# Kernel tuning notes

Measured on AMD Instinct MI355X. Metric: run time of the kernel, lower is better.

## Reference

```python
import jax, jax.numpy as jnp
import numpy as np


def setup_inputs() -> dict:
    key = jax.random.key(0)
    k1, k2, k3, k4 = jax.random.split(key, 4)
    B, N, dim, heads, dim_head = 4, 1025, 768, 12, 64
    inner = heads * dim_head
    x = jax.random.normal(k1, (B, N, dim), dtype=jnp.float32)
    # binary occlusion mask over the N-1 patch tokens (CLS handled inside forward)
    mask = (jax.random.uniform(k2, (B, N - 1, dim)) > 0.5).astype(jnp.float32)
    w_qkv = jax.random.normal(k3, (inner * 3, dim), dtype=jnp.float32) * 0.02
    w_out = jax.random.normal(k4, (dim, inner), dtype=jnp.float32) * 0.02
    b_out = jnp.zeros((dim,), dtype=jnp.float32)
    return {"x": x, "mask": mask, "w_qkv": w_qkv, "w_out": w_out, "b_out": b_out, "heads": heads}


def reference(x, mask, w_qkv, w_out, b_out, heads):
    B, N, dim = x.shape
    inner = w_qkv.shape[0] // 3
    d = inner // heads
    scale = d ** -0.5

    def split_heads(t):  # [B, n, h*d] -> [B, h, n, d]
        return t.reshape(B, t.shape[1], heads, d).transpose(0, 2, 1, 3)

    qkv = x @ w_qkv.T  # [B, N, 3*inner]
    q, k, v = map(split_heads, jnp.split(qkv, 3, axis=-1))

    # --- mask propagation (torch.no_grad block) ---
    mask_sg = jax.lax.stop_gradient(mask)
    qkv_m = mask_sg @ jax.lax.stop_gradient(jnp.abs(w_qkv)).T  # [B, N-1, 3*inner]

    def norm_mask(t):
        t = split_heads(t)  # [B, h, N-1, d]
        t = t / (1e-6 + jnp.max(t, axis=2, keepdims=True))
        return jnp.concatenate([jnp.ones_like(t[:, :, :1]), t], axis=2)  # [B, h, N, d]

    q_m, k_m, v_m = map(norm_mask, jnp.split(qkv_m, 3, axis=-1))
    updated = (jnp.mean(mask_sg, axis=-1, keepdims=True) > 0.0).astype(x.dtype)  # [B, N-1, 1]
    updated = jnp.concatenate([jnp.ones_like(updated[:, :1]), updated], axis=1)  # [B, N, 1]

    # --- masked attention ---
    dots = jnp.einsum('bhnd,bhmd->bhnm', q * q_m, k * k_m) * scale
    attn = jax.nn.softmax(dots, axis=-1)
    out = jnp.einsum('bhnm,bhmd->bhnd', attn, v_m * v)
    out = out.transpose(0, 2, 1, 3).reshape(B, N, inner) * updated
    out = out @ w_out.T + b_out

    # --- mask output propagation (no grad) ---
    m = jax.lax.stop_gradient(jnp.einsum('bhnm,bhmd->bhnd', attn, v_m))
    m = m.transpose(0, 2, 1, 3).reshape(B, N, inner) * updated
    m = m @ jax.lax.stop_gradient(jnp.abs(w_out)).T
    return (out, m[:, 1:])
```

## Files before the change

### kernel.cpp

```cpp
#include <hip/hip_runtime.h>
#include <cmath>

#define TPB 256

static const int NTOK  = 1025;
static const int DIM   = 768;
static const int HEADS = 12;
static const int QK3   = 2304;
static const int ROWS  = 4 * NTOK;
static const int MROWS = 4 * (NTOK - 1);
static const int MPAD  = 4224;
static const int NPAD  = 1088;
static const size_t OUT0 = (size_t)ROWS * DIM;
static const size_t APLANE = (size_t)MPAD * DIM;

static const size_t OFF_QKV16  = 0;
static const size_t OFF_QKVM16 = 4800000;
static const size_t OFF_QE     = 9600000;
static const size_t OFF_KF     = 11300000;
static const size_t OFF_VF     = 13000000;
static const size_t OFF_ABF    = 16400000;
static const size_t OFF_WQ     = 19700000;
static const size_t OFF_WO     = 21500000;
static const size_t OFF_CMAX   = 22100000;
static const size_t OFF_UPD    = 22110000;

typedef __attribute__((ext_vector_type(8))) short short8;
typedef __attribute__((ext_vector_type(4))) float f32x4;

__device__ __forceinline__ unsigned short f2bf(float f) {
    union { float f; unsigned int u; } c; c.f = f;
    unsigned int u = c.u + 0x7fffu + ((c.u >> 16) & 1u);
    return (unsigned short)(u >> 16);
}
__device__ __forceinline__ float bf2f(unsigned short u) {
    union { unsigned int u; float f; } c; c.u = (unsigned int)u << 16;
    return c.f;
}
__device__ __forceinline__ unsigned int cvtpk(float a, float b) {
    unsigned int r;
    asm("v_cvt_pk_bf16_f32 %0, %1, %2" : "=v"(r) : "v"(a), "v"(b));
    return r;
}
__device__ __forceinline__ void gl_lds16(const unsigned short* g, unsigned short* l) {
    __builtin_amdgcn_global_load_lds(
        (const __attribute__((address_space(1))) unsigned int*)g,
        (__attribute__((address_space(3))) unsigned int*)l, 16, 0, 0);
}

__global__ __launch_bounds__(TPB)
void k_cvt(const float* __restrict__ x, const float* __restrict__ mask,
           const float* __restrict__ wqkv, const float* __restrict__ wout,
           unsigned short* __restrict__ Abf, unsigned short* __restrict__ Wq,
           unsigned short* __restrict__ Wo, float* __restrict__ upd,
           float* __restrict__ cmax)
{
    const int z = blockIdx.z;
    if (z == 4) {
        const int bx = blockIdx.x;
        if (bx < 1025) {
            const int w = threadIdx.x >> 6, lane = threadIdx.x & 63;
            const int r = bx * 4 + w;
            if (r >= ROWS) return;
            const int b = r / NTOK, n = r % NTOK;
            float res = 1.f;
            if (n > 0) {
                const float* p = mask + (size_t)(b * (NTOK - 1) + (n - 1)) * DIM;
                float s = 0.f;
                for (int i = lane; i < DIM; i += 64) s += p[i];
#pragma unroll
                for (int off = 32; off > 0; off >>= 1) s += __shfl_xor(s, off, 64);
                res = (s > 0.f) ? 1.f : 0.f;
            }
            if (lane == 0) upd[r] = res;
        } else if (bx < 1034) {
            const int i4 = (bx - 1025) * 256 + threadIdx.x;
            *(float4*)(cmax + (size_t)i4 * 4) = (float4){0.f, 0.f, 0.f, 0.f};
        }
        return;
    }
    const size_t idx = ((size_t)blockIdx.x * TPB + threadIdx.x) * 8;
    unsigned short o[8] __attribute__((aligned(16)));
    if (z <= 1) {
        if (idx >= APLANE) return;
        const int row = (int)(idx / DIM);
        const int M = z ? MROWS : ROWS;
        const float* src = z ? mask : x;
        if (row < M) {
            float a[8];
            *(float4*)&a[0] = *(const float4*)(src + idx);
            *(float4*)&a[4] = *(const float4*)(src + idx + 4);
#pragma unroll
            for (int i = 0; i < 8; ++i) o[i] = f2bf(a[i]);
        } else {
#pragma unroll
            for (int i = 0; i < 8; ++i) o[i] = 0;
        }
        *(short8*)(Abf + (size_t)z * APLANE + idx) = *(short8*)o;
    } else {
        const size_t tot = (z == 2) ? (size_t)QK3 * DIM : (size_t)DIM * DIM;
        if (idx >= tot) return;
        const float* src = (z == 2) ? wqkv : wout;
        unsigned short* dst = (z == 2) ? Wq : Wo;
        float a[8];
        *(float4*)&a[0] = *(const float4*)(src + idx);
        *(float4*)&a[4] = *(const float4*)(src + idx + 4);
        unsigned short oa[8] __attribute__((aligned(16)));
#pragma unroll
        for (int i = 0; i < 8; ++i) { o[i] = f2bf(a[i]); oa[i] = f2bf(fabsf(a[i])); }
        *(short8*)(dst + idx) = *(short8*)o;
        *(short8*)(dst + tot + idx) = *(short8*)oa;
    }
}

__global__ __launch_bounds__(TPB)
void k_gemm_qkv_mfma(const unsigned short* __restrict__ Abf,
                     const unsigned short* __restrict__ Wq,
                     unsigned short* __restrict__ qkv16,
                     unsigned short* __restrict__ qkvm16,
                     float* __restrict__ cmax)
{
    const int bid = blockIdx.x;
    const int xcd = bid & 7, rr = bid >> 3;
    const int id = (xcd < 4) ? (xcd * 149 + rr) : (596 + (xcd - 4) * 148 + rr);
    const int z = id / 594;
    const int rem = id - z * 594;
    const int by = rem / 18, bx = rem - by * 18;
    const int rowT = by * 128, colT = bx * 128;
    if (z == 1 && rowT >= MROWS) return;
    const unsigned short* A = Abf + (size_t)z * APLANE;
    const unsigned short* B = Wq + (size_t)z * QK3 * DIM;

    __shared__ unsigned short As[2][128 * 64];
    __shared__ unsigned short Bs[2][128 * 64];

    const int t = threadIdx.x;
    const int w = t >> 6, lane = t & 63, l15 = lane & 15, quad = lane >> 4;
    const int wm = (w & 1) * 64, wn = (w >> 1) * 64;

    auto stage = [&](int buf, int k0) {
#pragma unroll
        for (int p = 0; p < 4; ++p) {
            const int i = p * 256 + t;
            const int row = i >> 3, ch = i & 7;
            const int gc = k0 + ((ch ^ (row & 7)) << 3);
            gl_lds16(A + (size_t)(rowT + row) * DIM + gc, As[buf] + (size_t)i * 8);
            gl_lds16(B + (size_t)(colT + row) * DIM + gc, Bs[buf] + (size_t)i * 8);
        }
    };

    f32x4 acc[4][4];
#pragma unroll
    for (int i = 0; i < 4; ++i)
#pragma unroll
        for (int j = 0; j < 4; ++j) acc[i][j] = (f32x4){0.f, 0.f, 0.f, 0.f};

    stage(0, 0);
#pragma clang loop unroll(disable)
    for (int kt = 0; kt < 12; ++kt) {
        const int cur = kt & 1;
        if (kt < 11) {
            stage(cur ^ 1, (kt + 1) * 64);
            asm volatile("s_waitcnt vmcnt(8)" ::: "memory");
        } else {
            asm volatile("s_waitcnt vmcnt(0)" ::: "memory");
        }
        __builtin_amdgcn_s_barrier();
        __builtin_amdgcn_sched_barrier(0);
        const unsigned short* as = As[cur];
        const unsigned short* bs = Bs[cur];
        short8 fa[2][4], fb[2][4];
#pragma unroll
        for (int kk = 0; kk < 2; ++kk) {
            const int rc = ((kk * 4 + quad) ^ (l15 & 7)) << 3;
#pragma unroll
            for (int mi = 0; mi < 4; ++mi) {
                fa[kk][mi] = *(const short8*)(as + (wm + mi * 16 + l15) * 64 + rc);
                fb[kk][mi] = *(const short8*)(bs + (wn + mi * 16 + l15) * 64 + rc);
            }
        }
        __builtin_amdgcn_s_setprio(1);
#pragma unroll
        for (int kk = 0; kk < 2; ++kk)
#pragma unroll
            for (int mi = 0; mi < 4; ++mi)
#pragma unroll
                for (int ni = 0; ni < 4; ++ni)
                    acc[mi][ni] = __builtin_amdgcn_mfma_f32_16x16x32_bf16(fa[kk][mi], fb[kk][ni], acc[mi][ni], 0, 0, 0);
        __builtin_amdgcn_s_setprio(0);
        asm volatile("s_waitcnt lgkmcnt(0)" ::: "memory");
        __builtin_amdgcn_s_barrier();
    }

    float cm[4] = {0.f, 0.f, 0.f, 0.f};
#pragma unroll
    for (int mi = 0; mi < 4; ++mi)
#pragma unroll
        for (int ni = 0; ni < 4; ++ni) {
            const int col = colT + wn + ni * 16 + l15;
#pragma unroll
            for (int r = 0; r < 4; ++r) {
                const int row = rowT + wm + mi * 16 + quad * 4 + r;
                const float v = acc[mi][ni][r];
                if (z == 0) {
                    if (row < ROWS) qkv16[(size_t)row * QK3 + col] = f2bf(v);
                } else {
                    qkvm16[(size_t)row * QK3 + col] = f2bf(v);
                    cm[ni] = fmaxf(cm[ni], v);
                }
            }
        }
    if (z == 1) {
        const int bb = rowT >> 10;
#pragma unroll
        for (int ni = 0; ni < 4; ++ni) {
            float m = cm[ni];
            m = fmaxf(m, __shfl_xor(m, 16, 64));
            m = fmaxf(m, __shfl_xor(m, 32, 64));
            if (quad == 0)
                atomicMax((int*)&cmax[bb * QK3 + colT + wn + ni * 16 + l15], __float_as_int(m));
        }
    }
}

__global__ __launch_bounds__(TPB)
void k_prep(const unsigned short* __restrict__ qkv16,
            const unsigned short* __restrict__ qkvm16,
            const float* __restrict__ cmax, unsigned short* __restrict__ qe,
            unsigned short* __restrict__ kfrag, unsigned short* __restrict__ vfrag)
{
    __shared__ unsigned short Vt_l[128 * 66];
    const int t = threadIdx.x;
    const int nt = blockIdx.x, h = blockIdx.y, b = blockIdx.z;
    const int bh = b * HEADS + h;
    const int nl = t >> 2, ds0 = (t & 3) * 16;
    const int n = nt * 64 + nl;
    const bool valid = n < NTOK;
    const int col0 = h * 64 + ds0;

    unsigned short q16[16] __attribute__((aligned(16))) = {0};
    unsigned short k16[16] __attribute__((aligned(16))) = {0};
    unsigned short v16[16] __attribute__((aligned(16))) = {0};
    unsigned short qm16[16] __attribute__((aligned(16)));
    unsigned short km16[16] __attribute__((aligned(16)));
    unsigned short vm16[16] __attribute__((aligned(16)));
    float cq[16], ck[16], cv[16];

    const bool useM = valid && (n > 0);
    if (valid) {
        const size_t br = (size_t)(b * NTOK + n) * QK3 + col0;
        *(short8*)&q16[0] = *(const short8*)(qkv16 + br);
        *(short8*)&q16[8] = *(const short8*)(qkv16 + br + 8);
        *(short8*)&k16[0] = *(const short8*)(qkv16 + br + 768);
        *(short8*)&k16[8] = *(const short8*)(qkv16 + br + 776);
        *(short8*)&v16[0] = *(const short8*)(qkv16 + br + 1536);
        *(short8*)&v16[8] = *(const short8*)(qkv16 + br + 1544);
    }
    if (useM) {
        const size_t mr = (size_t)(b * 1024 + (n - 1)) * QK3 + col0;
        *(short8*)&qm16[0] = *(const short8*)(qkvm16 + mr);
        *(short8*)&qm16[8] = *(const short8*)(qkvm16 + mr + 8);
        *(short8*)&km16[0] = *(const short8*)(qkvm16 + mr + 768);
        *(short8*)&km16[8] = *(const short8*)(qkvm16 + mr + 776);
        *(short8*)&vm16[0] = *(const short8*)(qkvm16 + mr + 1536);
        *(short8*)&vm16[8] = *(const short8*)(qkvm16 + mr + 1544);
        const int cb = b * QK3 + col0;
#pragma unroll
        for (int i = 0; i < 4; ++i) {
            *(float4*)&cq[i * 4] = *(const float4*)(cmax + cb + i * 4);
            *(float4*)&ck[i * 4] = *(const float4*)(cmax + cb + 768 + i * 4);
            *(float4*)&cv[i * 4] = *(const float4*)(cmax + cb + 1536 + i * 4);
        }
    }

    unsigned short oq[16] __attribute__((aligned(16)));
    unsigned short ok[16] __attribute__((aligned(16)));
#pragma unroll
    for (int idx = 0; idx < 16; ++idx) {
        const float qm = useM ? bf2f(qm16[idx]) / (1e-6f + cq[idx]) : 1.f;
        const float km = useM ? bf2f(km16[idx]) / (1e-6f + ck[idx]) : 1.f;
        const float vm = valid ? (useM ? bf2f(vm16[idx]) / (1e-6f + cv[idx]) : 1.f) : 0.f;
        oq[idx] = f2bf(bf2f(q16[idx]) * qm * 0.18033688f);
        ok[idx] = f2bf(bf2f(k16[idx]) * km);
        const int d = ds0 + idx;
        Vt_l[d * 66 + nl]        = f2bf(bf2f(v16[idx]) * vm);
        Vt_l[(64 + d) * 66 + nl] = f2bf(vm);
    }
    {
        unsigned short* qp = qe + ((size_t)bh * NPAD + n) * 64 + ds0;
        *(short8*)qp       = *(short8*)oq;
        *(short8*)(qp + 8) = *(short8*)(oq + 8);
    }
    {
        const int nc = nl >> 4, l15 = nl & 15;
        const int kk = ds0 >> 5, qb = (ds0 & 31) >> 3;
        unsigned short* kp = kfrag + (((size_t)bh * 17 + nt) * 8 + kk * 4 + nc) * 512;
        *(short8*)(kp + ((size_t)(qb * 16 + l15)) * 8)       = *(short8*)ok;
        *(short8*)(kp + ((size_t)((qb + 1) * 16 + l15)) * 8) = *(short8*)(ok + 8);
    }
    __syncthreads();
    const int c = t >> 1, nh = (t & 1) * 32;
    unsigned short ov[32] __attribute__((aligned(16)));
#pragma unroll
    for (int i = 0; i < 32; ++i) ov[i] = Vt_l[c * 66 + nh + i];
    const int c8 = c >> 4, l15v = c & 15, kkv = nh >> 5;
    unsigned short* vp = vfrag + (((size_t)bh * 17 + nt) * 16 + c8 * 2 + kkv) * 512 + (size_t)l15v * 8;
#pragma unroll
    for (int qd = 0; qd < 4; ++qd)
        *(short8*)(vp + (size_t)qd * 128) = *(short8*)(ov + qd * 8);
}

__global__ __launch_bounds__(64, 2)
void k_attn(const unsigned short* __restrict__ qe, const unsigned short* __restrict__ kfrag,
            const unsigned short* __restrict__ vfrag, const float* __restrict__ upd,
            unsigned short* __restrict__ ab2)
{
    const int flat = blockIdx.y * 33 + blockIdx.x;
    const int d2 = (flat & 7) * 198 + (flat >> 3);
    const int bh = d2 / 33, qt = d2 - bh * 33;
    const int b = bh / HEADS, h = bh - b * HEADS;
    const int lane = threadIdx.x;
    const int l15 = lane & 15, quad = lane >> 4;
    const int q0 = qt * 32;

    short8 qf[2][2];
#pragma unroll
    for (int j = 0; j < 2; ++j) {
        const unsigned short* qp = qe + ((size_t)bh * NPAD + q0 + j * 16 + l15) * 64 + (quad << 3);
        qf[j][0] = *(const short8*)qp;
        qf[j][1] = *(const short8*)(qp + 32);
    }
    const int pA = (quad & 1) * 32 + l15;
    const int pB = pA + 16;
    const bool lo32 = (lane < 32);

    const unsigned short* kb = kfrag + (size_t)bh * (17 * 8 * 512) + (size_t)lane * 8;
    const unsigned short* vb = vfrag + (size_t)bh * (17 * 16 * 512) + (size_t)lane * 8;

    short8 kf[8], vf[16];
#pragma unroll
    for (int g = 0; g < 8; ++g) kf[g] = *(const short8*)(kb + g * 512);
#pragma unroll
    for (int g = 0; g < 16; ++g) vf[g] = *(const short8*)(vb + g * 512);

    f32x4 acc[2][8];
    float lac[2] = {0.f, 0.f};
#pragma unroll
    for (int j = 0; j < 2; ++j)
#pragma unroll
        for (int g = 0; g < 8; ++g) acc[j][g] = (f32x4){0.f, 0.f, 0.f, 0.f};

    const float EC = 14.4269504f;

#pragma clang loop unroll(disable)
    for (int kt = 0; kt < 17; ++kt) {
        f32x4 s[2][4];
        __builtin_amdgcn_s_setprio(1);
#pragma unroll
        for (int nc = 0; nc < 4; ++nc) {
#pragma unroll
            for (int j = 0; j < 2; ++j) {
                f32x4 z = (f32x4){0.f, 0.f, 0.f, 0.f};
                z = __builtin_amdgcn_mfma_f32_16x16x32_bf16(kf[nc], qf[j][0], z, 0, 0, 0);
                z = __builtin_amdgcn_mfma_f32_16x16x32_bf16(kf[4 + nc], qf[j][1], z, 0, 0, 0);
                s[j][nc] = z;
            }
        }
        __builtin_amdgcn_s_setprio(0);
        if (kt < 16) {
            const unsigned short* kn = kb + (size_t)(kt + 1) * 4096;
#pragma unroll
            for (int g = 0; g < 8; ++g) kf[g] = *(const short8*)(kn + g * 512);
        }
        short8 pf[2][2];
#pragma unroll
        for (int j = 0; j < 2; ++j) {
            unsigned int dA[4], dB[4];
            float psum = 0.f, p00 = 0.f;
#pragma unroll
            for (int nc = 0; nc < 4; ++nc) {
                const float p0 = __builtin_amdgcn_exp2f(s[j][nc][0] - EC);
                const float p1 = __builtin_amdgcn_exp2f(s[j][nc][1] - EC);
                const float p2 = __builtin_amdgcn_exp2f(s[j][nc][2] - EC);
                const float p3 = __builtin_amdgcn_exp2f(s[j][nc][3] - EC);
                dA[nc] = cvtpk(p0, p1);
                dB[nc] = cvtpk(p2, p3);
                psum += (p0 + p1) + (p2 + p3);
                if (nc == 0) p00 = p0;
            }
            if (kt < 16) lac[j] += psum;
            else if (quad == 0) lac[j] += p00;
            union { int i[4]; short8 s; } u0, u1;
            {
                const int a0 = __shfl((int)dA[0], pA, 64), a1 = __shfl((int)dA[1], pA, 64);
                const int b0 = __shfl((int)dB[0], pA, 64), b1 = __shfl((int)dB[1], pA, 64);
                const int a2 = __shfl((int)dA[0], pB, 64), a3 = __shfl((int)dA[1], pB, 64);
                const int b2 = __shfl((int)dB[0], pB, 64), b3 = __shfl((int)dB[1], pB, 64);
                u0.i[0] = lo32 ? a0 : a1;
                u0.i[1] = lo32 ? b0 : b1;
                u0.i[2] = lo32 ? a2 : a3;
                u0.i[3] = lo32 ? b2 : b3;
            }
            {
                const int a0 = __shfl((int)dA[2], pA, 64), a1 = __shfl((int)dA[3], pA, 64);
                const int b0 = __shfl((int)dB[2], pA, 64), b1 = __shfl((int)dB[3], pA, 64);
                const int a2 = __shfl((int)dA[2], pB, 64), a3 = __shfl((int)dA[3], pB, 64);
                const int b2 = __shfl((int)dB[2], pB, 64), b3 = __shfl((int)dB[3], pB, 64);
                u1.i[0] = lo32 ? a0 : a1;
                u1.i[1] = lo32 ? b0 : b1;
                u1.i[2] = lo32 ? a2 : a3;
                u1.i[3] = lo32 ? b2 : b3;
            }
            pf[j][0] = u0.s;
            pf[j][1] = u1.s;
        }
        __builtin_amdgcn_s_setprio(1);
#pragma unroll
        for (int g = 0; g < 8; ++g) {
#pragma unroll
            for (int j = 0; j < 2; ++j) {
                acc[j][g] = __builtin_amdgcn_mfma_f32_16x16x32_bf16(vf[2 * g],     pf[j][0], acc[j][g], 0, 0, 0);
                acc[j][g] = __builtin_amdgcn_mfma_f32_16x16x32_bf16(vf[2 * g + 1], pf[j][1], acc[j][g], 0, 0, 0);
            }
        }
        __builtin_amdgcn_s_setprio(0);
        if (kt < 16) {
            const unsigned short* vn = vb + (size_t)(kt + 1) * 8192;
#pragma unroll
            for (int g = 0; g < 16; ++g) vf[g] = *(const short8*)(vn + g * 512);
        }
    }

#pragma unroll
    for (int j = 0; j < 2; ++j) {
        float lq = lac[j];
        lq += __shfl_xor(lq, 16, 64);
        lq += __shfl_xor(lq, 32, 64);
        const int qrow = q0 + j * 16 + l15;
        if (qrow < NTOK) {
            const size_t rg = (size_t)b * NTOK + qrow;
            const float inv = upd[rg] / lq;
#pragma unroll
            for (int g = 0; g < 8; ++g) {
                uint2 pk;
                pk.x = cvtpk(acc[j][g][0] * inv, acc[j][g][1] * inv);
                pk.y = cvtpk(acc[j][g][2] * inv, acc[j][g][3] * inv);
                const size_t addr = (size_t)(g >> 2) * APLANE + rg * DIM + h * 64 + (g & 3) * 16 + quad * 4;
                *(uint2*)(ab2 + addr) = pk;
            }
        }
    }
}

__global__ __launch_bounds__(TPB)
void k_gemm_out_mfma(const unsigned short* __restrict__ ab2,
                     const unsigned short* __restrict__ Wo,
                     const float* __restrict__ bout, float* __restrict__ dout)
{
    const int bid = blockIdx.x;
    const int xcd = bid & 7, rr = bid >> 3;
    const int id = (xcd < 4) ? (xcd * 50 + rr) : (200 + (xcd - 4) * 49 + rr);
    const int z = id / 198;
    const int rem = id - z * 198;
    const int by = rem / 6, bx = rem - by * 6;
    const int rowT = by * 128, colT = bx * 128;

    const unsigned short* A = ab2 + (size_t)z * APLANE;
    const unsigned short* B = Wo + (size_t)z * DIM * DIM;

    __shared__ unsigned short As[2][128 * 64];
    __shared__ unsigned short Bs[2][128 * 64];

    const int t = threadIdx.x;
    const int w = t >> 6, lane = t & 63, l15 = lane & 15, quad = lane >> 4;
    const int wm = (w & 1) * 64, wn = (w >> 1) * 64;

    auto stage = [&](int buf, int k0) {
#pragma unroll
        for (int p = 0; p < 4; ++p) {
            const int i = p * 256 + t;
            const int row = i >> 3, ch = i & 7;
            const int gc = k0 + ((ch ^ (row & 7)) << 3);
            gl_lds16(A + (size_t)(rowT + row) * DIM + gc, As[buf] + (size_t)i * 8);
            gl_lds16(B + (size_t)(colT + row) * DIM + gc, Bs[buf] + (size_t)i * 8);
        }
    };

    f32x4 acc[4][4];
#pragma unroll
    for (int i = 0; i < 4; ++i)
#pragma unroll
        for (int j = 0; j < 4; ++j) acc[i][j] = (f32x4){0.f, 0.f, 0.f, 0.f};

    stage(0, 0);
#pragma clang loop unroll(disable)
    for (int kt = 0; kt < 12; ++kt) {
        const int cur = kt & 1;
        if (kt < 11) {
            stage(cur ^ 1, (kt + 1) * 64);
            asm volatile("s_waitcnt vmcnt(8)" ::: "memory");
        } else {
            asm volatile("s_waitcnt vmcnt(0)" ::: "memory");
        }
        __builtin_amdgcn_s_barrier();
        __builtin_amdgcn_sched_barrier(0);
        const unsigned short* as = As[cur];
        const unsigned short* bs = Bs[cur];
        short8 fa[2][4], fb[2][4];
#pragma unroll
        for (int kk = 0; kk < 2; ++kk) {
            const int rc = ((kk * 4 + quad) ^ (l15 & 7)) << 3;
#pragma unroll
            for (int mi = 0; mi < 4; ++mi) {
                fa[kk][mi] = *(const short8*)(as + (wm + mi * 16 + l15) * 64 + rc);
                fb[kk][mi] = *(const short8*)(bs + (wn + mi * 16 + l15) * 64 + rc);
            }
        }
        __builtin_amdgcn_s_setprio(1);
#pragma unroll
        for (int kk = 0; kk < 2; ++kk)
#pragma unroll
            for (int mi = 0; mi < 4; ++mi)
#pragma unroll
                for (int ni = 0; ni < 4; ++ni)
                    acc[mi][ni] = __builtin_amdgcn_mfma_f32_16x16x32_bf16(fa[kk][mi], fb[kk][ni], acc[mi][ni], 0, 0, 0);
        __builtin_amdgcn_s_setprio(0);
        asm volatile("s_waitcnt lgkmcnt(0)" ::: "memory");
        __builtin_amdgcn_s_barrier();
    }

#pragma unroll
    for (int mi = 0; mi < 4; ++mi)
#pragma unroll
        for (int ni = 0; ni < 4; ++ni) {
            const int col = colT + wn + ni * 16 + l15;
            const float bb = (z == 0) ? bout[col] : 0.f;
#pragma unroll
            for (int r = 0; r < 4; ++r) {
                const int row = rowT + wm + mi * 16 + quad * 4 + r;
                if (row >= ROWS) continue;
                const int b = row / NTOK, n = row % NTOK;
                if (z == 0) {
                    dout[(size_t)row * DIM + col] = acc[mi][ni][r] + bb;
                } else if (n >= 1) {
                    dout[OUT0 + ((size_t)(b * (NTOK - 1) + (n - 1))) * DIM + col] = acc[mi][ni][r];
                }
            }
        }
}

extern "C" void kernel_launch(void* const* d_in, const int* in_sizes, int n_in,
                              void* d_out, int out_size, void* d_ws, size_t ws_size,
                              hipStream_t stream)
{
    const float* x    = (const float*)d_in[0];
    const float* mask = (const float*)d_in[1];
    const float* wqkv = (const float*)d_in[2];
    const float* wout = (const float*)d_in[3];
    const float* bout = (const float*)d_in[4];
    float* ws = (float*)d_ws;
    unsigned short* qkv16  = (unsigned short*)(ws + OFF_QKV16);
    unsigned short* qkvm16 = (unsigned short*)(ws + OFF_QKVM16);
    unsigned short* qe  = (unsigned short*)(ws + OFF_QE);
    unsigned short* kfr = (unsigned short*)(ws + OFF_KF);
    unsigned short* vfr = (unsigned short*)(ws + OFF_VF);
    unsigned short* abf = (unsigned short*)(ws + OFF_ABF);
    unsigned short* wq  = (unsigned short*)(ws + OFF_WQ);
    unsigned short* wo  = (unsigned short*)(ws + OFF_WO);
    float* cmax = ws + OFF_CMAX;
    float* upd  = ws + OFF_UPD;
    float* out  = (float*)d_out;

    hipLaunchKernelGGL(k_cvt,           dim3(1584, 1, 5), dim3(TPB), 0, stream, x, mask, wqkv, wout, abf, wq, wo, upd, cmax);
    hipLaunchKernelGGL(k_gemm_qkv_mfma, dim3(1188),       dim3(TPB), 0, stream, abf, wq, qkv16, qkvm16, cmax);
    hipLaunchKernelGGL(k_prep,          dim3(17, 12, 4),  dim3(TPB), 0, stream, qkv16, qkvm16, cmax, qe, kfr, vfr);
    hipLaunchKernelGGL(k_attn,          dim3(33, 48),     dim3(64),  0, stream, qe, kfr, vfr, upd, abf);
    hipLaunchKernelGGL(k_gemm_out_mfma, dim3(396),        dim3(TPB), 0, stream, abf, wo, bout, out);
}
```

Before: 214.8 us.

## Fold mask-row reduction into conversion, packed bf16 converts, narrower output GEMM tiles

The separate per-row mask reduction is removed. The conversion kernel now sets the row's update flag whenever an 8-element chunk of the mask sums positive, with the flag buffer cleared by a memset beforehand. This avoids rereading the mask. Float-to-bf16 conversions in the cvt and prep kernels use packed cvtpk, and the abs weight copy is made by clearing sign bits. The output GEMM tile shrinks from 128x128 to 128x64, doubling its grid to 792 blocks for better CU occupancy, with a simpler XCD mapping. The chunk-sum flag matches the row-mean test only because the mask is nonnegative, and the change adds concurrent racy stores of the same value plus an extra memset launch.

```diff
diff --git a/kernel.cpp b/kernel.cpp
--- a/kernel.cpp
+++ b/kernel.cpp
@@ -58,29 +58,16 @@
     const int z = blockIdx.z;
     if (z == 4) {
         const int bx = blockIdx.x;
-        if (bx < 1025) {
-            const int w = threadIdx.x >> 6, lane = threadIdx.x & 63;
-            const int r = bx * 4 + w;
-            if (r >= ROWS) return;
-            const int b = r / NTOK, n = r % NTOK;
-            float res = 1.f;
-            if (n > 0) {
-                const float* p = mask + (size_t)(b * (NTOK - 1) + (n - 1)) * DIM;
-                float s = 0.f;
-                for (int i = lane; i < DIM; i += 64) s += p[i];
-#pragma unroll
-                for (int off = 32; off > 0; off >>= 1) s += __shfl_xor(s, off, 64);
-                res = (s > 0.f) ? 1.f : 0.f;
-            }
-            if (lane == 0) upd[r] = res;
-        } else if (bx < 1034) {
-            const int i4 = (bx - 1025) * 256 + threadIdx.x;
+        if (bx == 0) {
+            if (threadIdx.x < 4) upd[threadIdx.x * NTOK] = 1.f;
+        } else if (bx < 10) {
+            const int i4 = (bx - 1) * 256 + threadIdx.x;
             *(float4*)(cmax + (size_t)i4 * 4) = (float4){0.f, 0.f, 0.f, 0.f};
         }
         return;
     }
     const size_t idx = ((size_t)blockIdx.x * TPB + threadIdx.x) * 8;
-    unsigned short o[8] __attribute__((aligned(16)));
+    union { unsigned int u[4]; short8 s; } pk;
     if (z <= 1) {
         if (idx >= APLANE) return;
         const int row = (int)(idx / DIM);
@@ -90,13 +77,19 @@
             float a[8];
             *(float4*)&a[0] = *(const float4*)(src + idx);
             *(float4*)&a[4] = *(const float4*)(src + idx + 4);
-#pragma unroll
-            for (int i = 0; i < 8; ++i) o[i] = f2bf(a[i]);
+            pk.u[0] = cvtpk(a[0], a[1]); pk.u[1] = cvtpk(a[2], a[3]);
+            pk.u[2] = cvtpk(a[4], a[5]); pk.u[3] = cvtpk(a[6], a[7]);
+            if (z == 1) {
+                const float s = ((a[0] + a[1]) + (a[2] + a[3])) + ((a[4] + a[5]) + (a[6] + a[7]));
+                if (s > 0.f) {
+                    const int b = row >> 10, j = row & 1023;
+                    upd[b * NTOK + j + 1] = 1.f;
+                }
+            }
         } else {
-#pragma unroll
-            for (int i = 0; i < 8; ++i) o[i] = 0;
-        }
-        *(short8*)(Abf + (size_t)z * APLANE + idx) = *(short8*)o;
+            pk.u[0] = pk.u[1] = pk.u[2] = pk.u[3] = 0u;
+        }
+        *(short8*)(Abf + (size_t)z * APLANE + idx) = pk.s;
     } else {
         const size_t tot = (z == 2) ? (size_t)QK3 * DIM : (size_t)DIM * DIM;
         if (idx >= tot) return;
@@ -105,11 +98,13 @@
         float a[8];
         *(float4*)&a[0] = *(const float4*)(src + idx);
         *(float4*)&a[4] = *(const float4*)(src + idx + 4);
-        unsigned short oa[8] __attribute__((aligned(16)));
-#pragma unroll
-        for (int i = 0; i < 8; ++i) { o[i] = f2bf(a[i]); oa[i] = f2bf(fabsf(a[i])); }
-        *(short8*)(dst + idx) = *(short8*)o;
-        *(short8*)(dst + tot + idx) = *(short8*)oa;
+        union { unsigned int u[4]; short8 s; } pa;
+        pk.u[0] = cvtpk(a[0], a[1]); pk.u[1] = cvtpk(a[2], a[3]);
+        pk.u[2] = cvtpk(a[4], a[5]); pk.u[3] = cvtpk(a[6], a[7]);
+#pragma unroll
+        for (int i = 0; i < 4; ++i) pa.u[i] = pk.u[i] & 0x7FFF7FFFu;
+        *(short8*)(dst + idx) = pk.s;
+        *(short8*)(dst + tot + idx) = pa.s;
     }
 }
 
@@ -273,30 +268,37 @@
         }
     }
 
-    unsigned short oq[16] __attribute__((aligned(16)));
-    unsigned short ok[16] __attribute__((aligned(16)));
+    float fq[16], fk[16];
 #pragma unroll
     for (int idx = 0; idx < 16; ++idx) {
         const float qm = useM ? bf2f(qm16[idx]) / (1e-6f + cq[idx]) : 1.f;
         const float km = useM ? bf2f(km16[idx]) / (1e-6f + ck[idx]) : 1.f;
         const float vm = valid ? (useM ? bf2f(vm16[idx]) / (1e-6f + cv[idx]) : 1.f) : 0.f;
-        oq[idx] = f2bf(bf2f(q16[idx]) * qm * 0.18033688f);
-        ok[idx] = f2bf(bf2f(k16[idx]) * km);
+        fq[idx] = bf2f(q16[idx]) * qm * 0.18033688f;
+        fk[idx] = bf2f(k16[idx]) * km;
         const int d = ds0 + idx;
         Vt_l[d * 66 + nl]        = f2bf(bf2f(v16[idx]) * vm);
         Vt_l[(64 + d) * 66 + nl] = f2bf(vm);
     }
+    union { unsigned int u[4]; short8 s; } pq0, pq1, pk0, pk1;
+#pragma unroll
+    for (int i = 0; i < 4; ++i) {
+        pq0.u[i] = cvtpk(fq[2 * i],     fq[2 * i + 1]);
+        pq1.u[i] = cvtpk(fq[8 + 2 * i], fq[9 + 2 * i]);
+        pk0.u[i] = cvtpk(fk[2 * i],     fk[2 * i + 1]);
+        pk1.u[i] = cvtpk(fk[8 + 2 * i], fk[9 + 2 * i]);
+    }
     {
         unsigned short* qp = qe + ((size_t)bh * NPAD + n) * 64 + ds0;
-        *(short8*)qp       = *(short8*)oq;
-        *(short8*)(qp + 8) = *(short8*)(oq + 8);
+        *(short8*)qp       = pq0.s;
+        *(short8*)(qp + 8) = pq1.s;
     }
     {
         const int nc = nl >> 4, l15 = nl & 15;
         const int kk = ds0 >> 5, qb = (ds0 & 31) >> 3;
         unsigned short* kp = kfrag + (((size_t)bh * 17 + nt) * 8 + kk * 4 + nc) * 512;
-        *(short8*)(kp + ((size_t)(qb * 16 + l15)) * 8)       = *(short8*)ok;
-        *(short8*)(kp + ((size_t)((qb + 1) * 16 + l15)) * 8) = *(short8*)(ok + 8);
+        *(short8*)(kp + ((size_t)(qb * 16 + l15)) * 8)       = pk0.s;
+        *(short8*)(kp + ((size_t)((qb + 1) * 16 + l15)) * 8) = pk1.s;
     }
     __syncthreads();
     const int c = t >> 1, nh = (t & 1) * 32;
@@ -459,21 +461,21 @@
 {
     const int bid = blockIdx.x;
     const int xcd = bid & 7, rr = bid >> 3;
-    const int id = (xcd < 4) ? (xcd * 50 + rr) : (200 + (xcd - 4) * 49 + rr);
-    const int z = id / 198;
-    const int rem = id - z * 198;
-    const int by = rem / 6, bx = rem - by * 6;
-    const int rowT = by * 128, colT = bx * 128;
+    const int id = xcd * 99 + rr;
+    const int z = id / 396;
+    const int rem = id - z * 396;
+    const int by = rem / 12, bx = rem - by * 12;
+    const int rowT = by * 128, colT = bx * 64;
 
     const unsigned short* A = ab2 + (size_t)z * APLANE;
     const unsigned short* B = Wo + (size_t)z * DIM * DIM;
 
     __shared__ unsigned short As[2][128 * 64];
-    __shared__ unsigned short Bs[2][128 * 64];
+    __shared__ unsigned short Bs[2][64 * 64];
 
     const int t = threadIdx.x;
     const int w = t >> 6, lane = t & 63, l15 = lane & 15, quad = lane >> 4;
-    const int wm = (w & 1) * 64, wn = (w >> 1) * 64;
+    const int wm = (w & 1) * 64, wn = (w >> 1) * 32;
 
     auto stage = [&](int buf, int k0) {
 #pragma unroll
@@ -482,15 +484,21 @@
             const int row = i >> 3, ch = i & 7;
             const int gc = k0 + ((ch ^ (row & 7)) << 3);
             gl_lds16(A + (size_t)(rowT + row) * DIM + gc, As[buf] + (size_t)i * 8);
+        }
+#pragma unroll
+        for (int p = 0; p < 2; ++p) {
+            const int i = p * 256 + t;
+            const int row = i >> 3, ch = i & 7;
+            const int gc = k0 + ((ch ^ (row & 7)) << 3);
             gl_lds16(B + (size_t)(colT + row) * DIM + gc, Bs[buf] + (size_t)i * 8);
         }
     };
 
-    f32x4 acc[4][4];
+    f32x4 acc[4][2];
 #pragma unroll
     for (int i = 0; i < 4; ++i)
 #pragma unroll
-        for (int j = 0; j < 4; ++j) acc[i][j] = (f32x4){0.f, 0.f, 0.f, 0.f};
+        for (int j = 0; j < 2; ++j) acc[i][j] = (f32x4){0.f, 0.f, 0.f, 0.f};
 
     stage(0, 0);
 #pragma clang loop unroll(disable)
@@ -498,7 +506,7 @@
         const int cur = kt & 1;
         if (kt < 11) {
             stage(cur ^ 1, (kt + 1) * 64);
-            asm volatile("s_waitcnt vmcnt(8)" ::: "memory");
+            asm volatile("s_waitcnt vmcnt(6)" ::: "memory");
         } else {
             asm volatile("s_waitcnt vmcnt(0)" ::: "memory");
         }
@@ -506,15 +514,16 @@
         __builtin_amdgcn_sched_barrier(0);
         const unsigned short* as = As[cur];
         const unsigned short* bs = Bs[cur];
-        short8 fa[2][4], fb[2][4];
+        short8 fa[2][4], fb[2][2];
 #pragma unroll
         for (int kk = 0; kk < 2; ++kk) {
             const int rc = ((kk * 4 + quad) ^ (l15 & 7)) << 3;
 #pragma unroll
-            for (int mi = 0; mi < 4; ++mi) {
+            for (int mi = 0; mi < 4; ++mi)
                 fa[kk][mi] = *(const short8*)(as + (wm + mi * 16 + l15) * 64 + rc);
-                fb[kk][mi] = *(const short8*)(bs + (wn + mi * 16 + l15) * 64 + rc);
-            }
+#pragma unroll
+            for (int ni = 0; ni < 2; ++ni)
+                fb[kk][ni] = *(const short8*)(bs + (wn + ni * 16 + l15) * 64 + rc);
         }
         __builtin_amdgcn_s_setprio(1);
 #pragma unroll
@@ -522,7 +531,7 @@
 #pragma unroll
             for (int mi = 0; mi < 4; ++mi)
 #pragma unroll
-                for (int ni = 0; ni < 4; ++ni)
+                for (int ni = 0; ni < 2; ++ni)
                     acc[mi][ni] = __builtin_amdgcn_mfma_f32_16x16x32_bf16(fa[kk][mi], fb[kk][ni], acc[mi][ni], 0, 0, 0);
         __builtin_amdgcn_s_setprio(0);
         asm volatile("s_waitcnt lgkmcnt(0)" ::: "memory");
@@ -532,7 +541,7 @@
 #pragma unroll
     for (int mi = 0; mi < 4; ++mi)
 #pragma unroll
-        for (int ni = 0; ni < 4; ++ni) {
+        for (int ni = 0; ni < 2; ++ni) {
             const int col = colT + wn + ni * 16 + l15;
             const float bb = (z == 0) ? bout[col] : 0.f;
 #pragma unroll
@@ -571,9 +580,10 @@
     float* upd  = ws + OFF_UPD;
     float* out  = (float*)d_out;
 
+    hipMemsetAsync(upd, 0, ROWS * sizeof(float), stream);
     hipLaunchKernelGGL(k_cvt,           dim3(1584, 1, 5), dim3(TPB), 0, stream, x, mask, wqkv, wout, abf, wq, wo, upd, cmax);
     hipLaunchKernelGGL(k_gemm_qkv_mfma, dim3(1188),       dim3(TPB), 0, stream, abf, wq, qkv16, qkvm16, cmax);
     hipLaunchKernelGGL(k_prep,          dim3(17, 12, 4),  dim3(TPB), 0, stream, qkv16, qkvm16, cmax, qe, kfr, vfr);
     hipLaunchKernelGGL(k_attn,          dim3(33, 48),     dim3(64),  0, stream, qe, kfr, vfr, upd, abf);
-    hipLaunchKernelGGL(k_gemm_out_mfma, dim3(396),        dim3(TPB), 0, stream, abf, wo, bout, out);
-}
+    hipLaunchKernelGGL(k_gemm_out_mfma, dim3(792),        dim3(TPB), 0, stream, abf, wo, bout, out);
+}
```

New measurement: 217.7 us. Within noise of the previous version (+1.4%).
